# Kernel optimization log

Measured on AMD Instinct MI355X. Metric: run time of the kernel, lower is better.

## Reference

```python
import jax, jax.numpy as jnp
import numpy as np

B, S, T, D, ST, C = 128, 37, 2048, 256, 8, 2  # batch, sensors, time, d_model, static, classes
MERGED = D + ST


def setup_inputs() -> dict:
    key = jax.random.key(0)
    ks = jax.random.split(key, 14)
    u = lambda k, shape, fan: jax.random.uniform(k, shape, jnp.float32, -1.0, 1.0) / np.sqrt(fan)
    return {
        "x": jax.random.normal(ks[0], (B, S, T), jnp.float32),
        "static": jax.random.normal(ks[1], (B, ST), jnp.float32),
        "time": jax.random.uniform(ks[2], (B, T), jnp.float32),
        "sensor_mask": jax.random.randint(ks[3], (B, S, T), 0, 2).astype(jnp.int32),
        # learned params (torch Linear stored here as [in, out])
        "W_sensor": u(ks[4], (2 * S, D), 2 * S),
        "b_sensor": u(ks[5], (D,), 2 * S),
        "W_time": u(ks[6], (1, D), 1),
        "b_time": u(ks[7], (D,), 1),
        "W_static": u(ks[8], (ST, ST), ST),
        "b_static": u(ks[9], (ST,), ST),
        "W_merge": u(ks[10], (MERGED, MERGED), MERGED),
        "b_merge": u(ks[11], (MERGED,), MERGED),
        "W_cls": u(ks[12], (MERGED, C), MERGED),
        "b_cls": u(ks[13], (C,), MERGED),
    }


def reference(x, static, time, sensor_mask, W_sensor, b_sensor, W_time, b_time,
              W_static, b_static, W_merge, b_merge, W_cls, b_cls):
    # [B,S,T] -> [B,T,S]; concat measurements with (float) sensor mask -> [B,T,2S]
    x_t = jnp.transpose(x, (0, 2, 1))
    m_t = jnp.transpose(sensor_mask, (0, 2, 1)).astype(jnp.float32)
    x_time = jnp.concatenate([x_t, m_t], axis=2)
    # timestep valid-mask: any nonzero feature at that step
    mask = (jnp.sum(x_time != 0, axis=2) > 0).astype(jnp.float32)  # [B,T]
    # sensor embedding + time encoding
    h = jnp.einsum('btf,fd->btd', x_time, W_sensor) + b_sensor
    h = h + time[..., None] * W_time[0] + b_time  # Linear(1, D) on time
    # NOTE: Mamba2ForCausalLM(vocab_size=0) produces logits with size(-1)==0,
    # so the original forward falls back to last_hidden_states = x_time (= h).
    # masked mean pooling over time
    denom = jnp.clip(jnp.sum(mask, axis=1), 1e-9)[:, None]  # [B,1]
    pooled = jnp.sum(h * mask[..., None], axis=1) / denom  # [B,D]
    static_e = static @ W_static + b_static  # [B,ST]
    comb = jnp.concatenate([pooled, static_e], axis=1)  # [B,MERGED]
    comb = jax.nn.relu(comb @ W_merge + b_merge)
    return comb @ W_cls + b_cls  # [B,C]
```

## Files before the change

### kernel.cpp

```cpp
#include <hip/hip_runtime.h>
#include <hip/hip_bf16.h>

#define BB   128
#define SS   37
#define TT   2048
#define DD   256
#define STT  8
#define CC   2
#define MER  264
#define FF   74

#define NC    4
#define CHUNK (TT / NC)
#define NJ    (CHUNK / 256)
#define RW    76
#define NW    8
#define NSW   5

__global__ __launch_bounds__(512) void reduce_kernel(
    const float* __restrict__ x,
    const int*   __restrict__ smk,
    const float* __restrict__ tarr,
    float* __restrict__ red)
{
    const int blk   = blockIdx.x;
    const int b     = blk >> 2;
    const int chunk = blk & 3;
    const int t0    = chunk * CHUNK;
    const int wave  = threadIdx.x >> 6;
    const int lane  = threadIdx.x & 63;

    float ax[NSW];
    float am[NSW];
    unsigned nz = 0;
#pragma unroll
    for (int i = 0; i < NSW; ++i) { ax[i] = 0.f; am[i] = 0.f; }

#pragma unroll
    for (int j = 0; j < NJ; ++j) {
        const int tb = t0 + 256 * j + 4 * lane;
#pragma unroll
        for (int si = 0; si < NSW; ++si) {
            const int s_raw = wave + NW * si;
            const int s     = (s_raw < SS) ? s_raw : (SS - 1);
            const size_t base = ((size_t)(b * SS + s)) * TT + tb;
            const float4 xv = *(const float4*)(x + base);
            const int4   mv = *(const int4*)(smk + base);
            const float sx = (xv.x + xv.y) + (xv.z + xv.w);
            const float sm = (float)((mv.x + mv.y) + (mv.z + mv.w));
            ax[si] += (s_raw < SS) ? sx : 0.f;
            am[si] += (s_raw < SS) ? sm : 0.f;
            unsigned f = (unsigned)((xv.x != 0.f) | (mv.x != 0))
                       | ((unsigned)((xv.y != 0.f) | (mv.y != 0)) << 1)
                       | ((unsigned)((xv.z != 0.f) | (mv.z != 0)) << 2)
                       | ((unsigned)((xv.w != 0.f) | (mv.w != 0)) << 3);
            nz |= f << (4 * j);
        }
    }

    __shared__ unsigned nzp[NW][64];
    nzp[wave][lane] = nz;
    __syncthreads();

    float* __restrict__ rrow = red + (size_t)blk * RW;

    if (wave == 0) {
        const unsigned m = (nzp[0][lane] | nzp[1][lane]) | (nzp[2][lane] | nzp[3][lane])
                         | (nzp[4][lane] | nzp[5][lane]) | (nzp[6][lane] | nzp[7][lane]);
        float cnt = 0.f, tsum = 0.f;
#pragma unroll
        for (int j = 0; j < NJ; ++j) {
            const float4 tv = *(const float4*)(tarr + (size_t)b * TT + t0 + 256 * j + 4 * lane);
            const unsigned mj = (m >> (4 * j)) & 0xFu;
            if (mj & 1u) { cnt += 1.f; tsum += tv.x; }
            if (mj & 2u) { cnt += 1.f; tsum += tv.y; }
            if (mj & 4u) { cnt += 1.f; tsum += tv.z; }
            if (mj & 8u) { cnt += 1.f; tsum += tv.w; }
        }
        for (int off = 32; off; off >>= 1) {
            cnt  += __shfl_down(cnt,  off, 64);
            tsum += __shfl_down(tsum, off, 64);
        }
        if (lane == 0) { rrow[74] = cnt; rrow[75] = tsum; }
    }

#pragma unroll
    for (int si = 0; si < NSW; ++si) {
        const int s_raw = wave + NW * si;
        float vx = ax[si], vm = am[si];
        for (int off = 32; off; off >>= 1) {
            vx += __shfl_down(vx, off, 64);
            vm += __shfl_down(vm, off, 64);
        }
        if (lane == 0 && s_raw < SS) { rrow[s_raw] = vx; rrow[SS + s_raw] = vm; }
    }
}

__global__ __launch_bounds__(320) void head_kernel(
    const float* __restrict__ red,
    const float* __restrict__ statics,
    const float* __restrict__ W_sensor,
    const float* __restrict__ b_sensor,
    const float* __restrict__ W_time,
    const float* __restrict__ b_time,
    const float* __restrict__ W_static,
    const float* __restrict__ b_static,
    const float* __restrict__ W_merge,
    const float* __restrict__ b_merge,
    const float* __restrict__ W_cls,
    const float* __restrict__ b_cls,
    float* __restrict__ out)
{
    const int b   = blockIdx.x;
    const int tid = threadIdx.x;

    __shared__ float sred[RW];
    __shared__ float comb[MER];
    __shared__ float comb2[MER];
    __shared__ float rbuf[10];

    if (tid < RW) {
        const float* rb = red + (size_t)b * NC * RW + tid;
        sred[tid] = (rb[0] + rb[RW]) + (rb[2 * RW] + rb[3 * RW]);
    }
    __syncthreads();

    const float smask = sred[74];
    const float stime = sred[75];
    const float inv   = 1.0f / fmaxf(smask, 1e-9f);

    if (tid < DD) {
        const int d = tid;
        float a0 = smask * (b_sensor[d] + b_time[d]) + stime * W_time[d];
        float a1 = 0.f;
#pragma unroll
        for (int f = 0; f < FF; f += 2) {
            a0 += sred[f]     * W_sensor[f * DD + d];
            a1 += sred[f + 1] * W_sensor[(f + 1) * DD + d];
        }
        comb[d] = (a0 + a1) * inv;
    } else if (tid < DD + STT) {
        const int j = tid - DD;
        float acc = b_static[j];
#pragma unroll
        for (int i = 0; i < STT; ++i)
            acc += statics[b * STT + i] * W_static[i * STT + j];
        comb[DD + j] = acc;
    }
    __syncthreads();

    if (tid < MER) {
        const int j = tid;
        float a[8];
#pragma unroll
        for (int k = 0; k < 8; ++k) a[k] = 0.f;
        for (int i = 0; i < MER; i += 8) {
#pragma unroll
            for (int k = 0; k < 8; ++k)
                a[k] += comb[i + k] * W_merge[(i + k) * MER + j];
        }
        const float acc = b_merge[j] +
            ((a[0] + a[1]) + (a[2] + a[3])) + ((a[4] + a[5]) + (a[6] + a[7]));
        comb2[j] = fmaxf(acc, 0.f);
    }
    __syncthreads();

    float c0 = 0.f, c1 = 0.f;
    if (tid < MER) {
        const float v = comb2[tid];
        c0 = v * W_cls[tid * CC];
        c1 = v * W_cls[tid * CC + 1];
    }
    for (int off = 32; off; off >>= 1) {
        c0 += __shfl_down(c0, off, 64);
        c1 += __shfl_down(c1, off, 64);
    }
    const int wv = tid >> 6, ln = tid & 63;
    if (ln == 0) { rbuf[wv] = c0; rbuf[5 + wv] = c1; }
    __syncthreads();
    if (tid == 0)
        out[b * CC + 0] = b_cls[0] + rbuf[0] + rbuf[1] + rbuf[2] + rbuf[3] + rbuf[4];
    if (tid == 1)
        out[b * CC + 1] = b_cls[1] + rbuf[5] + rbuf[6] + rbuf[7] + rbuf[8] + rbuf[9];
}

extern "C" void kernel_launch(void* const* d_in, const int* in_sizes, int n_in,
                              void* d_out, int out_size, void* d_ws, size_t ws_size,
                              hipStream_t stream) {
    const float* x        = (const float*)d_in[0];
    const float* statics  = (const float*)d_in[1];
    const float* tarr     = (const float*)d_in[2];
    const int*   smk      = (const int*)  d_in[3];
    const float* W_sensor = (const float*)d_in[4];
    const float* b_sensor = (const float*)d_in[5];
    const float* W_time   = (const float*)d_in[6];
    const float* b_time   = (const float*)d_in[7];
    const float* W_static = (const float*)d_in[8];
    const float* b_static = (const float*)d_in[9];
    const float* W_merge  = (const float*)d_in[10];
    const float* b_merge  = (const float*)d_in[11];
    const float* W_cls    = (const float*)d_in[12];
    const float* b_cls    = (const float*)d_in[13];
    float* out = (float*)d_out;
    float* red = (float*)d_ws;

    reduce_kernel<<<BB * NC, 512, 0, stream>>>(x, smk, tarr, red);
    head_kernel<<<BB, 320, 0, stream>>>(red, statics, W_sensor, b_sensor,
                                        W_time, b_time, W_static, b_static,
                                        W_merge, b_merge, W_cls, b_cls, out);
}
```

Before: 138.6 us.

## Fuse reduction and head kernels via per-batch atomic counter and spin-wait

Merges the time-reduction kernel and the MLP head kernel into one launch. Every block bumps a per-batch atomic counter after writing its partial sums. The chunk-0 block for each batch then spin-waits until all four partials have arrived and runs the head computation inline. This aims to remove the second kernel launch and its dependency gap. In exchange it adds a memset launch for the counters and a spin-wait that holds a block on its CU, which relies on all blocks being co-resident.

Result: slower. 319.6 us (+130.6%).

```diff
diff --git a/kernel.cpp b/kernel.cpp
--- a/kernel.cpp
+++ b/kernel.cpp
@@ -17,18 +17,34 @@
 #define NW    8
 #define NSW   5
 
-__global__ __launch_bounds__(512) void reduce_kernel(
+#define RED_BYTES (BB * NC * RW * 4)
+
+__global__ __launch_bounds__(512, 4) void fused_kernel(
     const float* __restrict__ x,
     const int*   __restrict__ smk,
     const float* __restrict__ tarr,
-    float* __restrict__ red)
+    const float* __restrict__ statics,
+    const float* __restrict__ W_sensor,
+    const float* __restrict__ b_sensor,
+    const float* __restrict__ W_time,
+    const float* __restrict__ b_time,
+    const float* __restrict__ W_static,
+    const float* __restrict__ b_static,
+    const float* __restrict__ W_merge,
+    const float* __restrict__ b_merge,
+    const float* __restrict__ W_cls,
+    const float* __restrict__ b_cls,
+    float* __restrict__ red,
+    unsigned* __restrict__ cnt,
+    float* __restrict__ out)
 {
     const int blk   = blockIdx.x;
     const int b     = blk >> 2;
     const int chunk = blk & 3;
     const int t0    = chunk * CHUNK;
-    const int wave  = threadIdx.x >> 6;
-    const int lane  = threadIdx.x & 63;
+    const int tid   = threadIdx.x;
+    const int wave  = tid >> 6;
+    const int lane  = tid & 63;
 
     float ax[NSW];
     float am[NSW];
@@ -67,21 +83,21 @@
     if (wave == 0) {
         const unsigned m = (nzp[0][lane] | nzp[1][lane]) | (nzp[2][lane] | nzp[3][lane])
                          | (nzp[4][lane] | nzp[5][lane]) | (nzp[6][lane] | nzp[7][lane]);
-        float cnt = 0.f, tsum = 0.f;
+        float cntv = 0.f, tsum = 0.f;
 #pragma unroll
         for (int j = 0; j < NJ; ++j) {
             const float4 tv = *(const float4*)(tarr + (size_t)b * TT + t0 + 256 * j + 4 * lane);
             const unsigned mj = (m >> (4 * j)) & 0xFu;
-            if (mj & 1u) { cnt += 1.f; tsum += tv.x; }
-            if (mj & 2u) { cnt += 1.f; tsum += tv.y; }
-            if (mj & 4u) { cnt += 1.f; tsum += tv.z; }
-            if (mj & 8u) { cnt += 1.f; tsum += tv.w; }
+            if (mj & 1u) { cntv += 1.f; tsum += tv.x; }
+            if (mj & 2u) { cntv += 1.f; tsum += tv.y; }
+            if (mj & 4u) { cntv += 1.f; tsum += tv.z; }
+            if (mj & 8u) { cntv += 1.f; tsum += tv.w; }
         }
         for (int off = 32; off; off >>= 1) {
-            cnt  += __shfl_down(cnt,  off, 64);
+            cntv += __shfl_down(cntv, off, 64);
             tsum += __shfl_down(tsum, off, 64);
         }
-        if (lane == 0) { rrow[74] = cnt; rrow[75] = tsum; }
+        if (lane == 0) { rrow[74] = cntv; rrow[75] = tsum; }
     }
 
 #pragma unroll
@@ -94,30 +110,25 @@
         }
         if (lane == 0 && s_raw < SS) { rrow[s_raw] = vx; rrow[SS + s_raw] = vm; }
     }
-}
-
-__global__ __launch_bounds__(320) void head_kernel(
-    const float* __restrict__ red,
-    const float* __restrict__ statics,
-    const float* __restrict__ W_sensor,
-    const float* __restrict__ b_sensor,
-    const float* __restrict__ W_time,
-    const float* __restrict__ b_time,
-    const float* __restrict__ W_static,
-    const float* __restrict__ b_static,
-    const float* __restrict__ W_merge,
-    const float* __restrict__ b_merge,
-    const float* __restrict__ W_cls,
-    const float* __restrict__ b_cls,
-    float* __restrict__ out)
-{
-    const int b   = blockIdx.x;
-    const int tid = threadIdx.x;
+
+    __threadfence();
+    __syncthreads();
+    if (tid == 0) atomicAdd(&cnt[b], 1u);
+
+    if (chunk != 0) return;
+
+    if (tid == 0) {
+        while (__hip_atomic_load(&cnt[b], __ATOMIC_RELAXED, __HIP_MEMORY_SCOPE_AGENT) < 4u)
+            __builtin_amdgcn_s_sleep(2);
+        __threadfence();
+    }
+    __syncthreads();
+    __threadfence();
 
     __shared__ float sred[RW];
     __shared__ float comb[MER];
     __shared__ float comb2[MER];
-    __shared__ float rbuf[10];
+    __shared__ float rbuf[16];
 
     if (tid < RW) {
         const float* rb = red + (size_t)b * NC * RW + tid;
@@ -175,13 +186,14 @@
         c0 += __shfl_down(c0, off, 64);
         c1 += __shfl_down(c1, off, 64);
     }
-    const int wv = tid >> 6, ln = tid & 63;
-    if (ln == 0) { rbuf[wv] = c0; rbuf[5 + wv] = c1; }
+    if (lane == 0) { rbuf[wave] = c0; rbuf[8 + wave] = c1; }
     __syncthreads();
     if (tid == 0)
-        out[b * CC + 0] = b_cls[0] + rbuf[0] + rbuf[1] + rbuf[2] + rbuf[3] + rbuf[4];
+        out[b * CC + 0] = b_cls[0] + rbuf[0] + rbuf[1] + rbuf[2] + rbuf[3]
+                        + rbuf[4] + rbuf[5] + rbuf[6] + rbuf[7];
     if (tid == 1)
-        out[b * CC + 1] = b_cls[1] + rbuf[5] + rbuf[6] + rbuf[7] + rbuf[8] + rbuf[9];
+        out[b * CC + 1] = b_cls[1] + rbuf[8] + rbuf[9] + rbuf[10] + rbuf[11]
+                        + rbuf[12] + rbuf[13] + rbuf[14] + rbuf[15];
 }
 
 extern "C" void kernel_launch(void* const* d_in, const int* in_sizes, int n_in,
@@ -203,9 +215,12 @@
     const float* b_cls    = (const float*)d_in[13];
     float* out = (float*)d_out;
     float* red = (float*)d_ws;
-
-    reduce_kernel<<<BB * NC, 512, 0, stream>>>(x, smk, tarr, red);
-    head_kernel<<<BB, 320, 0, stream>>>(red, statics, W_sensor, b_sensor,
-                                        W_time, b_time, W_static, b_static,
-                                        W_merge, b_merge, W_cls, b_cls, out);
+    unsigned* cnt = (unsigned*)((char*)d_ws + RED_BYTES);
+
+    (void)hipMemsetAsync(cnt, 0, BB * sizeof(unsigned), stream);
+
+    fused_kernel<<<BB * NC, 512, 0, stream>>>(x, smk, tarr, statics,
+                                              W_sensor, b_sensor, W_time, b_time,
+                                              W_static, b_static, W_merge, b_merge,
+                                              W_cls, b_cls, red, cnt, out);
 }
```
